# Kernel optimization log

Measured on AMD Instinct MI355X. Metric: run time of the kernel, lower is better.

The kernel has to match this reference:

```python
import jax, jax.numpy as jnp
import numpy as np

N_NODES = 10000
N_EDGES = 50000
N_GRAPHS = 64
NODE_DIM = 32
EDGE_DIM = 16
HID = 64
EDGE_HID = 128
OUT_DIM = 1
T_STEPS = 3       # message-passing rounds
S2S_STEPS = 6     # Set2Set processing steps


def setup_inputs() -> dict:
    key = jax.random.key(0)
    ks = jax.random.split(key, 24)
    def w(k, shape, scale):
        return (jax.random.normal(k, shape, dtype=jnp.float32) * scale)
    inp = {}
    inp["node_features"] = jax.random.normal(ks[0], (N_NODES, NODE_DIM), dtype=jnp.float32)
    inp["edge_features"] = jax.random.normal(ks[1], (N_EDGES, EDGE_DIM), dtype=jnp.float32)
    inp["edge_index"] = jax.random.randint(ks[2], (2, N_EDGES), 0, N_NODES, dtype=jnp.int32)
    # sorted, fully-covering graph assignment (nodes of each graph are contiguous)
    inp["batch_indices"] = ((jnp.arange(N_NODES) * N_GRAPHS) // N_NODES).astype(jnp.int32)
    # input projection
    inp["W_proj"] = w(ks[3], (NODE_DIM, HID), 1.0 / np.sqrt(NODE_DIM))
    inp["b_proj"] = jnp.zeros((HID,), jnp.float32)
    # edge network MLP: edge_dim -> edge_hid -> hid*hid
    inp["W_e1"] = w(ks[4], (EDGE_DIM, EDGE_HID), 1.0 / np.sqrt(EDGE_DIM))
    inp["b_e1"] = jnp.zeros((EDGE_HID,), jnp.float32)
    inp["W_e2"] = w(ks[5], (EDGE_HID, HID * HID), 0.01)
    inp["b_e2"] = jnp.zeros((HID * HID,), jnp.float32)
    # GRU cell (torch layout: 3*hid rows = r,z,n)
    inp["W_gih"] = w(ks[6], (3 * HID, HID), 1.0 / np.sqrt(HID))
    inp["W_ghh"] = w(ks[7], (3 * HID, HID), 1.0 / np.sqrt(HID))
    inp["b_gih"] = jnp.zeros((3 * HID,), jnp.float32)
    inp["b_ghh"] = jnp.zeros((3 * HID,), jnp.float32)
    # LSTM cell (torch layout: 4*hid rows = i,f,g,o), input 2*hid
    inp["W_lih"] = w(ks[8], (4 * HID, 2 * HID), 1.0 / np.sqrt(HID))
    inp["W_lhh"] = w(ks[9], (4 * HID, HID), 1.0 / np.sqrt(HID))
    inp["b_lih"] = jnp.zeros((4 * HID,), jnp.float32)
    inp["b_lhh"] = jnp.zeros((4 * HID,), jnp.float32)
    # readout MLP: 2*hid -> hid -> out
    inp["W_m1"] = w(ks[10], (2 * HID, HID), 1.0 / np.sqrt(2 * HID))
    inp["b_m1"] = jnp.zeros((HID,), jnp.float32)
    inp["W_m2"] = w(ks[11], (HID, OUT_DIM), 1.0 / np.sqrt(HID))
    inp["b_m2"] = jnp.zeros((OUT_DIM,), jnp.float32)
    return inp


def _scatter_softmax(e, idx, n_seg):
    mx = jax.ops.segment_max(e, idx, num_segments=n_seg)
    ex = jnp.exp(e - mx[idx])
    s = jax.ops.segment_sum(ex, idx, num_segments=n_seg)
    return ex / (s[idx] + 1e-16)


def _mpnn_forward(node_features, edge_features, edge_index, batch_indices,
                  W_proj, b_proj, W_e1, b_e1, W_e2, b_e2,
                  W_gih, W_ghh, b_gih, b_ghh,
                  W_lih, W_lhh, b_lih, b_lhh,
                  W_m1, b_m1, W_m2, b_m2):
    n_nodes = node_features.shape[0]
    dst = edge_index[0]  # receiving node v
    src = edge_index[1]  # sending node w

    # input projection
    h = node_features @ W_proj + b_proj                       # (N, H)

    # edge network: per-edge transformation matrix A(e_vw) (depends only on edge feats)
    A = jax.nn.relu(edge_features @ W_e1 + b_e1) @ W_e2 + b_e2
    A = A.reshape(-1, HID, HID)                               # (E, H, H)

    # T rounds: gather senders, per-edge bmm, scatter-add to receivers, GRU update
    for _ in range(T_STEPS):
        msgs = jnp.einsum('eij,ej->ei', A, h[src])            # (E, H)
        m = jax.ops.segment_sum(msgs, dst, num_segments=n_nodes)
        gx = m @ W_gih.T + b_gih                              # (N, 3H)
        gh = h @ W_ghh.T + b_ghh
        xr, xz, xn = jnp.split(gx, 3, axis=-1)
        hr, hz, hn = jnp.split(gh, 3, axis=-1)
        r = jax.nn.sigmoid(xr + hr)
        z = jax.nn.sigmoid(xz + hz)
        n = jnp.tanh(xn + r * hn)
        h = (1.0 - z) * n + z * h

    # Set2Set readout
    hs = jnp.zeros((N_GRAPHS, HID), h.dtype)
    cs = jnp.zeros((N_GRAPHS, HID), h.dtype)
    rs = jnp.zeros((N_GRAPHS, HID), h.dtype)
    for _ in range(S2S_STEPS):
        q = hs[batch_indices]                                 # (N, H)
        e = jnp.sum(h * q, axis=-1)                           # (N,)
        a = _scatter_softmax(e, batch_indices, N_GRAPHS)
        rs = jax.ops.segment_sum(a[:, None] * h, batch_indices, num_segments=N_GRAPHS)
        x = jnp.concatenate([hs, rs], axis=-1)                # (G, 2H)
        gates = x @ W_lih.T + b_lih + hs @ W_lhh.T + b_lhh    # (G, 4H)
        i, f, g, o = jnp.split(gates, 4, axis=-1)
        cs = jax.nn.sigmoid(f) * cs + jax.nn.sigmoid(i) * jnp.tanh(g)
        hs = jax.nn.sigmoid(o) * jnp.tanh(cs)
    ge = jnp.concatenate([hs, rs], axis=-1)                   # (G, 2H)
    return jax.nn.relu(ge @ W_m1 + b_m1) @ W_m2 + b_m2        # (G, out)


def reference(node_features, edge_features, edge_index, batch_indices,
              W_proj, b_proj, W_e1, b_e1, W_e2, b_e2,
              W_gih, W_ghh, b_gih, b_ghh,
              W_lih, W_lhh, b_lih, b_lhh,
              W_m1, b_m1, W_m2, b_m2):
    return _mpnn_forward(node_features, edge_features, edge_index, batch_indices,
                         W_proj, b_proj, W_e1, b_e1, W_e2, b_e2,
                         W_gih, W_ghh, b_gih, b_ghh,
                         W_lih, W_lhh, b_lih, b_lhh,
                         W_m1, b_m1, W_m2, b_m2)
```

## Files before the change

### kernel.cpp

```cpp
#include <hip/hip_runtime.h>

#define N_NODES   10000
#define N_EDGES   50000
#define N_GRAPHS  64
#define NODE_DIM  32
#define EDGE_DIM  16
#define HID       64
#define EHID      128
#define T_STEPS   3
#define S2S_STEPS 6

typedef _Float16 half_t;
typedef _Float16 f16x8 __attribute__((ext_vector_type(8)));
typedef float    f32x4 __attribute__((ext_vector_type(4)));

__device__ __forceinline__ float sigf(float x){ return 1.0f/(1.0f + expf(-x)); }

__global__ void k_zero(float* p, int n){
  int i = blockIdx.x*256 + threadIdx.x;
  if (i < n) p[i] = 0.0f;
}

__global__ void k_proj(const float* __restrict__ nf, const float* __restrict__ Wp,
                       const float* __restrict__ bp, float* __restrict__ h){
  int idx = blockIdx.x*256 + threadIdx.x;
  if (idx >= N_NODES*HID) return;
  int n = idx >> 6;
  int c = idx & 63;
  float acc = bp[c];
  const float* row = nf + (size_t)n*NODE_DIM;
  for (int j = 0; j < NODE_DIM; ++j)
    acc = fmaf(row[j], Wp[j*HID + c], acc);
  h[idx] = acc;
}

__global__ void k_tw2(const float* __restrict__ W2, float* __restrict__ Mm){
  int idx = blockIdx.x*256 + threadIdx.x;
  if (idx >= 64*8192) return;
  int j = idx >> 13; int o = idx & 8191; int k = o >> 6; int i = o & 63;
  Mm[idx] = W2[(size_t)k*4096 + i*64 + j];
}

__global__ void k_w2bt(const float* __restrict__ W2, half_t* __restrict__ BT){
  int idx = blockIdx.x*256 + threadIdx.x;
  if (idx >= 512*2*64*8) return;
  int j    = idx & 7;
  int lane = (idx >> 3) & 63;
  int tk   = (idx >> 9) & 1;
  int tn   = idx >> 10;
  int k = tk*32 + ((lane >> 4) << 3) + j;
  int o = tn*16 + (lane & 15);
  BT[idx] = (half_t)W2[(size_t)(o >> 6)*4096 + (o & 63)*64 + k];
}

__global__ void k_h2a(const float* __restrict__ h, half_t* __restrict__ AT){
  int idx = blockIdx.x*256 + threadIdx.x;
  if (idx >= 625*2*64*8) return;
  int j    = idx & 7;
  int lane = (idx >> 3) & 63;
  int tk   = (idx >> 9) & 1;
  int tm   = idx >> 10;
  int mrow = tm*16 + (lane & 15);
  int k    = tk*32 + ((lane >> 4) << 3) + j;
  AT[idx] = (half_t)h[(size_t)mrow*64 + k];
}

__global__ void k_prep(const float* __restrict__ h, const float* __restrict__ be2,
                       float* __restrict__ m, float* __restrict__ bhp,
                       half_t* __restrict__ AT){
  int idx = blockIdx.x*256 + threadIdx.x;
  if (idx >= N_NODES*HID) return;
  m[idx] = 0.0f;
  int n = idx >> 6, i = idx & 63;
  float acc = 0.0f;
  const float* row = be2 + (size_t)i*64;
  const float* hr  = h + (size_t)n*64;
  for (int j = 0; j < 64; ++j)
    acc = fmaf(row[j], hr[j], acc);
  bhp[idx] = acc;
  int j    = idx & 7;
  int lane = (idx >> 3) & 63;
  int tk   = (idx >> 9) & 1;
  int tm   = idx >> 10;
  int mrow = tm*16 + (lane & 15);
  int k    = tk*32 + ((lane >> 4) << 3) + j;
  AT[idx] = (half_t)h[(size_t)mrow*64 + k];
}

__global__ void k_twg(const float* __restrict__ Wg, const float* __restrict__ Wh,
                      float* __restrict__ WgT, float* __restrict__ WhT){
  int idx = blockIdx.x*256 + threadIdx.x;
  if (idx >= 192*64) return;
  int row = idx >> 6;
  int j   = idx & 63;
  WgT[j*192 + row] = Wg[(size_t)row*64 + j];
  WhT[j*192 + row] = Wh[(size_t)row*64 + j];
}

__global__ void k_ehid(const float* __restrict__ ef, const float* __restrict__ W1,
                       const float* __restrict__ b1, float* __restrict__ Hid){
  int idx = blockIdx.x*256 + threadIdx.x;
  if (idx >= N_EDGES*EHID) return;
  int e = idx >> 7, c = idx & 127;
  float acc = b1[c];
  const float* er = ef + (size_t)e*EDGE_DIM;
  for (int j = 0; j < EDGE_DIM; ++j)
    acc = fmaf(er[j], W1[j*EHID + c], acc);
  Hid[idx] = fmaxf(acc, 0.0f);
}

__global__ void k_ehid16(const float* __restrict__ ef, const float* __restrict__ W1,
                         const float* __restrict__ b1, half_t* __restrict__ Hid16){
  int idx = blockIdx.x*256 + threadIdx.x;
  if (idx >= N_EDGES*EHID) return;
  int e = idx >> 7, c = idx & 127;
  float acc = b1[c];
  const float* er = ef + (size_t)e*EDGE_DIM;
  for (int j = 0; j < EDGE_DIM; ++j)
    acc = fmaf(er[j], W1[j*EHID + c], acc);
  Hid16[idx] = (half_t)fmaxf(acc, 0.0f);
}

__global__ void k_bh(const float* __restrict__ h, const float* __restrict__ be2,
                     float* __restrict__ bh){
  int idx = blockIdx.x*256 + threadIdx.x;
  if (idx >= N_NODES*HID) return;
  int n = idx >> 6, i = idx & 63;
  float acc = 0.0f;
  const float* row = be2 + (size_t)i*64;
  const float* hr  = h + (size_t)n*64;
  for (int j = 0; j < 64; ++j)
    acc = fmaf(row[j], hr[j], acc);
  bh[idx] = acc;
}

__global__ void k_hist(const int* __restrict__ ei, int* __restrict__ deg){
  int e = blockIdx.x*256 + threadIdx.x;
  if (e >= N_EDGES) return;
  atomicAdd(&deg[ei[N_EDGES + e]], 1);
}

__global__ void k_scan(const int* __restrict__ deg, int* __restrict__ rowptr,
                       int* __restrict__ cursor){
  __shared__ int part[256];
  int t = threadIdx.x;
  int base = t*40;
  int s = 0;
  for (int i = 0; i < 40; ++i){
    int idx = base + i;
    if (idx < N_NODES) s += deg[idx];
  }
  part[t] = s;
  __syncthreads();
  for (int off = 1; off < 256; off <<= 1){
    int v = (t >= off) ? part[t - off] : 0;
    __syncthreads();
    part[t] += v;
    __syncthreads();
  }
  int run = (t > 0) ? part[t - 1] : 0;
  for (int i = 0; i < 40; ++i){
    int idx = base + i;
    if (idx < N_NODES){
      rowptr[idx] = run;
      cursor[idx] = run;
      run += deg[idx];
    }
  }
  if (t == 255) rowptr[N_NODES] = run;
}

__global__ void k_scatter(const int* __restrict__ ei, int* __restrict__ cursor,
                          int* __restrict__ csr){
  int e = blockIdx.x*256 + threadIdx.x;
  if (e >= N_EDGES) return;
  int src = ei[N_EDGES + e];
  int pos = atomicAdd(&cursor[src], 1);
  csr[pos] = e;
}

__global__ void MPNN_55705725829535_kernel(const half_t* __restrict__ AT,
                                           const half_t* __restrict__ BT,
                                           const int* __restrict__ rowptr,
                                           const int* __restrict__ csr,
                                           const int* __restrict__ ei,
                                           const half_t* __restrict__ Hid16,
                                           const float* __restrict__ bh,
                                           float* __restrict__ m){
  __shared__ half_t Ct[8][4][520];
  __shared__ int dstW[4][16];
  int wv   = threadIdx.x >> 6;
  int lane = threadIdx.x & 63;
  int quad = lane >> 4;
  int colb = lane & 15;
  int tmb = blockIdx.x;
  int q   = blockIdx.y;
  int tile = tmb >> 1;
  int hi   = tmb & 1;

  int srcl = (lane & 48) | (hi << 3) | (lane & 7);
  const f16x8* Ab = (const f16x8*)AT + (size_t)tile*128;
  f16x8 a0 = Ab[srcl];
  f16x8 a1 = Ab[64 + srcl];
  #pragma unroll
  for (int kt = 0; kt < 4; ++kt){
    f32x4 acc[8];
    #pragma unroll
    for (int jj = 0; jj < 8; ++jj){
      acc[jj][0]=0.f; acc[jj][1]=0.f; acc[jj][2]=0.f; acc[jj][3]=0.f;
    }
    #pragma unroll
    for (int jj = 0; jj < 8; ++jj){
      int ke = kt*32 + wv*8 + jj;
      int tn = ke*4 + q;
      const f16x8* Bb = (const f16x8*)BT + (size_t)tn*128;
      acc[jj] = __builtin_amdgcn_mfma_f32_16x16x32_f16(a0, Bb[lane],      acc[jj], 0, 0, 0);
      acc[jj] = __builtin_amdgcn_mfma_f32_16x16x32_f16(a1, Bb[64 + lane], acc[jj], 0, 0, 0);
    }
    if (quad < 2){
      #pragma unroll
      for (int r = 0; r < 4; ++r){
        int node = quad*4 + r;
        f16x8 v;
        #pragma unroll
        for (int jj = 0; jj < 8; ++jj) v[jj] = (half_t)acc[jj][r];
        *(f16x8*)&Ct[node][kt][(wv*16 + colb)*8] = v;
      }
    }
  }
  __syncthreads();

  for (int c = 0; c < 2; ++c){
    int node = wv*2 + c;
    int s = tmb*8 + node;
    int beg  = rowptr[s];
    int endp = rowptr[s + 1];
    if (beg == endp) continue;
    f16x8 B[4];
    #pragma unroll
    for (int kt = 0; kt < 4; ++kt)
      B[kt] = *(const f16x8*)&Ct[node][kt][lane*8];
    float bhc = bh[(size_t)s*64 + q*16 + colb];
    for (int gbeg = beg; gbeg < endp; gbeg += 16){
      int gn = endp - gbeg; if (gn > 16) gn = 16;
      if (lane < 16)
        dstW[wv][lane] = (lane < gn) ? ei[csr[gbeg + lane]] : -1;
      f16x8 A[4];
      if (colb < gn){
        int e = csr[gbeg + colb];
        const f16x8* Hb = (const f16x8*)(Hid16 + (size_t)e*128) + quad;
        #pragma unroll
        for (int kt = 0; kt < 4; ++kt)
          A[kt] = Hb[kt*4];
      } else {
        #pragma unroll
        for (int kt = 0; kt < 4; ++kt)
          #pragma unroll
          for (int p = 0; p < 8; ++p) A[kt][p] = (half_t)0;
      }
      f32x4 acc;
      acc[0]=0.f; acc[1]=0.f; acc[2]=0.f; acc[3]=0.f;
      #pragma unroll
      for (int kt = 0; kt < 4; ++kt)
        acc = __builtin_amdgcn_mfma_f32_16x16x32_f16(A[kt], B[kt], acc, 0, 0, 0);
      #pragma unroll
      for (int r = 0; r < 4; ++r){
        int jrow = quad*4 + r;
        if (jrow < gn){
          int d = dstW[wv][jrow];
          atomicAdd(&m[(size_t)d*64 + q*16 + colb], acc[r] + bhc);
        }
      }
    }
  }
}

__global__ void k_cgemm(const float* __restrict__ h, const float* __restrict__ Mm,
                        half_t* __restrict__ C, int lo, int hi){
  __shared__ float hs[16][64];
  int n0 = lo + blockIdx.x*16;
  int o0 = blockIdx.y*256 + threadIdx.x;
  for (int idx = threadIdx.x; idx < 16*64; idx += 256){
    int nn = idx >> 6, j = idx & 63;
    int node = n0 + nn;
    hs[nn][j] = (node < hi) ? h[(size_t)node*64 + j] : 0.0f;
  }
  __syncthreads();
  float acc0[16], acc1[16];
  #pragma unroll
  for (int nn = 0; nn < 16; ++nn){ acc0[nn] = 0.0f; acc1[nn] = 0.0f; }
  for (int j4 = 0; j4 < 16; ++j4){
    const float* M0 = Mm + (size_t)(j4*4)*8192;
    float a0 = M0[o0],            b0 = M0[o0 + 4096];
    float a1 = M0[8192 + o0],     b1 = M0[8192 + o0 + 4096];
    float a2 = M0[2*8192 + o0],   b2 = M0[2*8192 + o0 + 4096];
    float a3 = M0[3*8192 + o0],   b3 = M0[3*8192 + o0 + 4096];
    #pragma unroll
    for (int nn = 0; nn < 16; ++nn){
      float4 hv = *(const float4*)&hs[nn][j4*4];
      acc0[nn] = fmaf(hv.x, a0, acc0[nn]);
      acc1[nn] = fmaf(hv.x, b0, acc1[nn]);
      acc0[nn] = fmaf(hv.y, a1, acc0[nn]);
      acc1[nn] = fmaf(hv.y, b1, acc1[nn]);
      acc0[nn] = fmaf(hv.z, a2, acc0[nn]);
      acc1[nn] = fmaf(hv.z, b2, acc1[nn]);
      acc0[nn] = fmaf(hv.w, a3, acc0[nn]);
      acc1[nn] = fmaf(hv.w, b3, acc1[nn]);
    }
  }
  #pragma unroll
  for (int nn = 0; nn < 16; ++nn){
    int node = n0 + nn;
    if (node < hi){
      half_t* Cr = C + (size_t)(node - lo)*8192;
      Cr[o0]        = (half_t)acc0[nn];
      Cr[o0 + 4096] = (half_t)acc1[nn];
    }
  }
}

__global__ void k_msg_csr(const int* __restrict__ rowptr,
                          const int* __restrict__ csr,
                          const int* __restrict__ ei,
                          const float* __restrict__ Hid,
                          const half_t* __restrict__ C,
                          const float* __restrict__ bh,
                          float* __restrict__ m, int lo, int hi){
  __shared__ float hidL[4][8][128];
  int wave = threadIdx.x >> 6;
  int lane = threadIdx.x & 63;
  int s = lo + blockIdx.x*4 + wave;
  if (s >= hi) return;
  int beg = rowptr[s];
  int endp = rowptr[s + 1];
  if (beg == endp) return;
  float bhv = bh[(size_t)s*64 + lane];
  const half_t* Cb = C + (size_t)(s - lo)*8192 + lane;
  float (*hl)[128] = hidL[wave];
  for (int gbeg = beg; gbeg < endp; gbeg += 8){
    int gn = endp - gbeg; if (gn > 8) gn = 8;
    int dsts[8];
    int e0 = csr[gbeg];
    #pragma unroll
    for (int j = 0; j < 8; ++j){
      int e = (j < gn) ? csr[gbeg + j] : e0;
      dsts[j] = ei[e];
      hl[j][lane]      = Hid[(size_t)e*128 + lane];
      hl[j][lane + 64] = Hid[(size_t)e*128 + 64 + lane];
    }
    float acc[8];
    #pragma unroll
    for (int j = 0; j < 8; ++j) acc[j] = 0.0f;
    #pragma unroll 4
    for (int k = 0; k < 128; ++k){
      float c = (float)Cb[k*64];
      #pragma unroll
      for (int j = 0; j < 8; ++j)
        acc[j] = fmaf(hl[j][k], c, acc[j]);
    }
    for (int j = 0; j < gn; ++j)
      atomicAdd(&m[(size_t)dsts[j]*64 + lane], acc[j] + bhv);
  }
}

__global__ void k_msg_fb(const int* __restrict__ ei, const float* __restrict__ ef,
                         const float* __restrict__ W1, const float* __restrict__ b1,
                         const float* __restrict__ W2, const float* __restrict__ be2,
                         const float* __restrict__ h, float* __restrict__ m){
  __shared__ float HidL[EHID];
  __shared__ __align__(16) float hsL[HID];
  int e = blockIdx.x;
  int t = threadIdx.x;
  int src = ei[N_EDGES + e];
  int dst = ei[e];
  {
    float a0 = b1[t];
    float a1 = b1[t + 64];
    const float* er = ef + (size_t)e*EDGE_DIM;
    for (int j = 0; j < EDGE_DIM; ++j){
      float ev = er[j];
      a0 = fmaf(ev, W1[j*EHID + t],      a0);
      a1 = fmaf(ev, W1[j*EHID + t + 64], a1);
    }
    HidL[t]      = fmaxf(a0, 0.0f);
    HidL[t + 64] = fmaxf(a1, 0.0f);
    hsL[t] = h[(size_t)src*64 + t];
  }
  __syncthreads();
  float acc = 0.0f;
  for (int k = 0; k < EHID; ++k){
    float s = HidL[k];
    if (s != 0.0f){
      const float* w = W2 + (size_t)k*4096 + t*64;
      float partial = 0.0f;
      for (int j = 0; j < 64; ++j)
        partial = fmaf(hsL[j], w[j], partial);
      acc = fmaf(s, partial, acc);
    }
  }
  {
    const float* w = be2 + (size_t)t*64;
    for (int j = 0; j < 64; ++j)
      acc = fmaf(hsL[j], w[j], acc);
  }
  atomicAdd(&m[(size_t)dst*64 + t], acc);
}

__global__ void k_gru(float* __restrict__ h, const float* __restrict__ m,
                      const float* __restrict__ WgT, const float* __restrict__ WhT,
                      const float* __restrict__ bg, const float* __restrict__ bhb){
  __shared__ float mld[16][64];
  __shared__ float hld[16][64];
  int t  = threadIdx.x;
  int i  = t & 63;
  int wv = t >> 6;
  int n0 = blockIdx.x*16;
  for (int idx = t; idx < 16*64; idx += 256){
    int nn = idx >> 6, j = idx & 63;
    int node = n0 + nn;
    mld[nn][j] = m[(size_t)node*64 + j];
    hld[nn][j] = h[(size_t)node*64 + j];
  }
  __syncthreads();
  float xr[4], xz[4], xn[4], hr[4], hz[4], hn[4];
  #pragma unroll
  for (int c = 0; c < 4; ++c){
    xr[c] = bg[i];  xz[c] = bg[64 + i];  xn[c] = bg[128 + i];
    hr[c] = bhb[i]; hz[c] = bhb[64 + i]; hn[c] = bhb[128 + i];
  }
  for (int j = 0; j < 64; ++j){
    const float* wg = WgT + j*192;
    const float* wh = WhT + j*192;
    float wgr = wg[i], wgz = wg[64 + i], wgn = wg[128 + i];
    float whr = wh[i], whz = wh[64 + i], whn = wh[128 + i];
    #pragma unroll
    for (int c = 0; c < 4; ++c){
      int nn = wv*4 + c;
      float mj = mld[nn][j];
      float hj = hld[nn][j];
      xr[c] = fmaf(mj, wgr, xr[c]);
      xz[c] = fmaf(mj, wgz, xz[c]);
      xn[c] = fmaf(mj, wgn, xn[c]);
      hr[c] = fmaf(hj, whr, hr[c]);
      hz[c] = fmaf(hj, whz, hz[c]);
      hn[c] = fmaf(hj, whn, hn[c]);
    }
  }
  #pragma unroll
  for (int c = 0; c < 4; ++c){
    int nn = wv*4 + c;
    float r  = sigf(xr[c] + hr[c]);
    float z  = sigf(xz[c] + hz[c]);
    float nv = tanhf(xn[c] + r*hn[c]);
    h[(size_t)(n0 + nn)*64 + i] = (1.0f - z)*nv + z*hld[nn][i];
  }
}

__global__ void k_s2s(const float* __restrict__ h,
                      const float* __restrict__ Wli, const float* __restrict__ Wlh,
                      const float* __restrict__ bli, const float* __restrict__ blh,
                      const float* __restrict__ Wm1, const float* __restrict__ bm1,
                      const float* __restrict__ Wm2, const float* __restrict__ bm2,
                      float* __restrict__ out){
  __shared__ float hc[157*65];
  __shared__ float ea[160];
  __shared__ float x[192];
  __shared__ float gpart[512];
  __shared__ float rsp[8][64];
  __shared__ float wredA[8];
  __shared__ float wredB[8];
  __shared__ float hsb[64];
  __shared__ float csb[64];
  __shared__ float rsb[64];
  int g = blockIdx.x;
  int t = threadIdx.x;
  int lane = t & 63;
  int wv   = t >> 6;
  int start = (g*N_NODES + 63) >> 6;
  int end   = ((g + 1)*N_NODES + 63) >> 6;
  int cnt = end - start;
  const float* hg = h + (size_t)start*64;
  for (int idx = t; idx < cnt*64; idx += 512)
    hc[(idx >> 6)*65 + (idx & 63)] = hg[idx];
  if (t < 64){ hsb[t] = 0.0f; csb[t] = 0.0f; rsb[t] = 0.0f; }
  __syncthreads();
  for (int step = 0; step < S2S_STEPS; ++step){
    float ev = -1e30f;
    if (t < cnt){
      float a = 0.0f;
      const float* hr = &hc[t*65];
      for (int i = 0; i < 64; ++i) a = fmaf(hr[i], hsb[i], a);
      ev = a;
    }
    float v = ev;
    for (int o = 32; o > 0; o >>= 1) v = fmaxf(v, __shfl_xor(v, o));
    if (lane == 0) wredA[wv] = v;
    __syncthreads();
    float mx = wredA[0];
    #pragma unroll
    for (int i = 1; i < 8; ++i) mx = fmaxf(mx, wredA[i]);
    float ex = (t < cnt) ? expf(ev - mx) : 0.0f;
    float sv = ex;
    for (int o = 32; o > 0; o >>= 1) sv += __shfl_xor(sv, o);
    if (lane == 0) wredB[wv] = sv;
    __syncthreads();
    float ssum = 0.0f;
    #pragma unroll
    for (int i = 0; i < 8; ++i) ssum += wredB[i];
    if (t < cnt) ea[t] = ex / (ssum + 1e-16f);
    __syncthreads();
    {
      int n0 = wv*20;
      int n1 = n0 + 20; if (n1 > cnt) n1 = cnt;
      float r = 0.0f;
      for (int n = n0; n < n1; ++n)
        r = fmaf(ea[n], hc[n*65 + lane], r);
      rsp[wv][lane] = r;
    }
    __syncthreads();
    if (t < 64){
      float r = rsp[0][t] + rsp[1][t] + rsp[2][t] + rsp[3][t]
              + rsp[4][t] + rsp[5][t] + rsp[6][t] + rsp[7][t];
      rsb[t] = r;
      x[t]        = hsb[t];
      x[64 + t]   = r;
      x[128 + t]  = hsb[t];
    }
    __syncthreads();
    {
      int gate = t & 255;
      int half = t >> 8;
      float gl = 0.0f;
      if (half == 0){
        const float* wr = Wli + (size_t)gate*128;
        for (int jj = 0; jj < 96; ++jj) gl = fmaf(x[jj], wr[jj], gl);
      } else {
        const float* wr = Wli + (size_t)gate*128;
        for (int jj = 96; jj < 128; ++jj) gl = fmaf(x[jj], wr[jj], gl);
        const float* wh = Wlh + (size_t)gate*64;
        for (int jj = 0; jj < 64; ++jj) gl = fmaf(x[128 + jj], wh[jj], gl);
      }
      gpart[t] = gl;
    }
    __syncthreads();
    if (t < 64){
      float iv = sigf (gpart[t]       + gpart[t + 256]       + bli[t]       + blh[t]);
      float fv = sigf (gpart[64 + t]  + gpart[64 + t + 256]  + bli[64 + t]  + blh[64 + t]);
      float gv = tanhf(gpart[128 + t] + gpart[128 + t + 256] + bli[128 + t] + blh[128 + t]);
      float ov = sigf (gpart[192 + t] + gpart[192 + t + 256] + bli[192 + t] + blh[192 + t]);
      float c  = fv*csb[t] + iv*gv;
      csb[t] = c;
      hsb[t] = ov*tanhf(c);
    }
    __syncthreads();
  }
  float rv = 0.0f;
  if (t < 64){
    float v = bm1[t];
    for (int j = 0; j < 64; ++j) v = fmaf(hsb[j], Wm1[(size_t)j*64 + t],        v);
    for (int j = 0; j < 64; ++j) v = fmaf(rsb[j], Wm1[(size_t)(64 + j)*64 + t], v);
    v = fmaxf(v, 0.0f);
    rv = v * Wm2[t];
  }
  for (int o = 32; o > 0; o >>= 1) rv += __shfl_xor(rv, o);
  if (lane == 0) wredA[wv] = rv;
  __syncthreads();
  if (t == 0) out[g] = wredA[0] + wredA[1] + wredA[2] + wredA[3]
                     + wredA[4] + wredA[5] + wredA[6] + wredA[7] + bm2[0];
}

extern "C" void kernel_launch(void* const* d_in, const int* in_sizes, int n_in,
                              void* d_out, int out_size, void* d_ws, size_t ws_size,
                              hipStream_t stream){
  (void)in_sizes; (void)n_in; (void)out_size;

  const float* nf  = (const float*)d_in[0];
  const float* ef  = (const float*)d_in[1];
  const int*   ei  = (const int*)d_in[2];
  const float* Wp  = (const float*)d_in[4];
  const float* bp  = (const float*)d_in[5];
  const float* We1 = (const float*)d_in[6];
  const float* be1 = (const float*)d_in[7];
  const float* We2 = (const float*)d_in[8];
  const float* be2 = (const float*)d_in[9];
  const float* Wg  = (const float*)d_in[10];
  const float* Wh  = (const float*)d_in[11];
  const float* bg  = (const float*)d_in[12];
  const float* bhb = (const float*)d_in[13];
  const float* Wli = (const float*)d_in[14];
  const float* Wlh = (const float*)d_in[15];
  const float* bli = (const float*)d_in[16];
  const float* blh = (const float*)d_in[17];
  const float* Wm1 = (const float*)d_in[18];
  const float* bm1 = (const float*)d_in[19];
  const float* Wm2 = (const float*)d_in[20];
  const float* bm2 = (const float*)d_in[21];

  float* out = (float*)d_out;
  float* ws  = (float*)d_ws;

  float* h    = ws;
  float* m    = ws + 640000;
  float* bh   = ws + 1280000;
  float* Mm   = ws + 1920000;
  float* WgT  = ws + 2444288;
  float* WhT  = ws + 2456576;
  float* Hid  = ws + 2468864;
  half_t* Hid16 = (half_t*)Hid;
  int*   deg    = (int*)(ws + 8868864);
  int*   rowptr = deg + 10000;
  int*   cursor = rowptr + 10001;
  int*   csr    = cursor + 10000;
  half_t* AT  = (half_t*)(ws + 8948880);
  half_t* BT  = (half_t*)(ws + 9268880);
  const size_t C_OFF = 9531024;
  half_t* C   = (half_t*)(ws + C_OFF);

  long long c_halves = ((long long)ws_size - (long long)C_OFF*4) / 2;
  int NC = (c_halves > 0) ? (int)(c_halves / 8192) : 0;
  if (NC > N_NODES) NC = N_NODES;
  int use_c_path = (NC >= 512);
  int use_mfma   = (NC >= N_NODES);

  k_proj<<<(N_NODES*HID + 255)/256, 256, 0, stream>>>(nf, Wp, bp, h);

  if (use_c_path){
    k_twg <<<(192*64 + 255)/256, 256, 0, stream>>>(Wg, Wh, WgT, WhT);
    k_zero<<<(10000 + 255)/256, 256, 0, stream>>>((float*)deg, 10000);
    k_hist<<<(N_EDGES + 255)/256, 256, 0, stream>>>(ei, deg);
    k_scan<<<1, 256, 0, stream>>>(deg, rowptr, cursor);
    k_scatter<<<(N_EDGES + 255)/256, 256, 0, stream>>>(ei, cursor, csr);
    if (use_mfma){
      k_ehid16<<<(N_EDGES*EHID + 255)/256, 256, 0, stream>>>(ef, We1, be1, Hid16);
      k_w2bt<<<(512*2*64*8 + 255)/256, 256, 0, stream>>>(We2, BT);
      for (int step = 0; step < T_STEPS; ++step){
        k_prep<<<(N_NODES*HID + 255)/256, 256, 0, stream>>>(h, be2, m, bh, AT);
        dim3 grid(1250, 4);
        MPNN_55705725829535_kernel<<<grid, 256, 0, stream>>>(
            AT, BT, rowptr, csr, ei, Hid16, bh, m);
        k_gru<<<625, 256, 0, stream>>>(h, m, WgT, WhT, bg, bhb);
      }
    } else {
      k_ehid<<<(N_EDGES*EHID + 255)/256, 256, 0, stream>>>(ef, We1, be1, Hid);
      k_tw2<<<(64*8192)/256, 256, 0, stream>>>(We2, Mm);
      for (int step = 0; step < T_STEPS; ++step){
        k_zero<<<(N_NODES*HID + 255)/256, 256, 0, stream>>>(m, N_NODES*HID);
        k_bh<<<(N_NODES*HID + 255)/256, 256, 0, stream>>>(h, be2, bh);
        for (int lo = 0; lo < N_NODES; lo += NC){
          int hi = (lo + NC < N_NODES) ? lo + NC : N_NODES;
          int cnt = hi - lo;
          dim3 grid((cnt + 15)/16, 16);
          k_cgemm<<<grid, 256, 0, stream>>>(h, Mm, C, lo, hi);
          k_msg_csr<<<(cnt + 3)/4, 256, 0, stream>>>(
              rowptr, csr, ei, Hid, C, bh, m, lo, hi);
        }
        k_gru<<<625, 256, 0, stream>>>(h, m, WgT, WhT, bg, bhb);
      }
    }
  } else {
    k_twg <<<(192*64 + 255)/256, 256, 0, stream>>>(Wg, Wh, WgT, WhT);
    for (int step = 0; step < T_STEPS; ++step){
      k_zero<<<(N_NODES*HID + 255)/256, 256, 0, stream>>>(m, N_NODES*HID);
      k_msg_fb<<<N_EDGES, 64, 0, stream>>>(ei, ef, We1, be1, We2, be2, h, m);
      k_gru<<<625, 256, 0, stream>>>(h, m, WgT, WhT, bg, bhb);
    }
  }
  k_s2s<<<N_GRAPHS, 512, 0, stream>>>(h, Wli, Wlh, bli, blh,
                                      Wm1, bm1, Wm2, bm2, out);
}
```

Before: 582.6 us.

## Split message kernel over K halves, using full 16-node MFMA tiles per block

```diff
diff --git a/kernel.cpp b/kernel.cpp
--- a/kernel.cpp
+++ b/kernel.cpp
@@ -187,23 +187,22 @@
                                            const half_t* __restrict__ Hid16,
                                            const float* __restrict__ bh,
                                            float* __restrict__ m){
-  __shared__ half_t Ct[8][4][520];
+  __shared__ half_t Ct[16][2][520];
   __shared__ int dstW[4][16];
   int wv   = threadIdx.x >> 6;
   int lane = threadIdx.x & 63;
   int quad = lane >> 4;
   int colb = lane & 15;
-  int tmb = blockIdx.x;
-  int q   = blockIdx.y;
-  int tile = tmb >> 1;
-  int hi   = tmb & 1;
-
-  int srcl = (lane & 48) | (hi << 3) | (lane & 7);
-  const f16x8* Ab = (const f16x8*)AT + (size_t)tile*128;
-  f16x8 a0 = Ab[srcl];
-  f16x8 a1 = Ab[64 + srcl];
+  int tm = blockIdx.x;
+  int q  = blockIdx.y;
+  int kh = blockIdx.z;
+
+  const f16x8* Ab = (const f16x8*)AT + (size_t)tm*128;
+  f16x8 a0 = Ab[lane];
+  f16x8 a1 = Ab[64 + lane];
   #pragma unroll
-  for (int kt = 0; kt < 4; ++kt){
+  for (int ktl = 0; ktl < 2; ++ktl){
+    int kt = kh*2 + ktl;
     f32x4 acc[8];
     #pragma unroll
     for (int jj = 0; jj < 8; ++jj){
@@ -217,52 +216,44 @@
       acc[jj] = __builtin_amdgcn_mfma_f32_16x16x32_f16(a0, Bb[lane],      acc[jj], 0, 0, 0);
       acc[jj] = __builtin_amdgcn_mfma_f32_16x16x32_f16(a1, Bb[64 + lane], acc[jj], 0, 0, 0);
     }
-    if (quad < 2){
+    #pragma unroll
+    for (int r = 0; r < 4; ++r){
+      int node = quad*4 + r;
+      f16x8 v;
       #pragma unroll
-      for (int r = 0; r < 4; ++r){
-        int node = quad*4 + r;
-        f16x8 v;
-        #pragma unroll
-        for (int jj = 0; jj < 8; ++jj) v[jj] = (half_t)acc[jj][r];
-        *(f16x8*)&Ct[node][kt][(wv*16 + colb)*8] = v;
-      }
+      for (int jj = 0; jj < 8; ++jj) v[jj] = (half_t)acc[jj][r];
+      *(f16x8*)&Ct[node][ktl][(wv*16 + colb)*8] = v;
     }
   }
   __syncthreads();
 
-  for (int c = 0; c < 2; ++c){
-    int node = wv*2 + c;
-    int s = tmb*8 + node;
+  for (int c = 0; c < 4; ++c){
+    int node = wv*4 + c;
+    int s = tm*16 + node;
     int beg  = rowptr[s];
     int endp = rowptr[s + 1];
     if (beg == endp) continue;
-    f16x8 B[4];
-    #pragma unroll
-    for (int kt = 0; kt < 4; ++kt)
-      B[kt] = *(const f16x8*)&Ct[node][kt][lane*8];
-    float bhc = bh[(size_t)s*64 + q*16 + colb];
+    f16x8 B0 = *(const f16x8*)&Ct[node][0][lane*8];
+    f16x8 B1 = *(const f16x8*)&Ct[node][1][lane*8];
+    float bhc = (kh == 0) ? bh[(size_t)s*64 + q*16 + colb] : 0.0f;
     for (int gbeg = beg; gbeg < endp; gbeg += 16){
       int gn = endp - gbeg; if (gn > 16) gn = 16;
       if (lane < 16)
         dstW[wv][lane] = (lane < gn) ? ei[csr[gbeg + lane]] : -1;
-      f16x8 A[4];
+      f16x8 A0, A1;
       if (colb < gn){
         int e = csr[gbeg + colb];
         const f16x8* Hb = (const f16x8*)(Hid16 + (size_t)e*128) + quad;
-        #pragma unroll
-        for (int kt = 0; kt < 4; ++kt)
-          A[kt] = Hb[kt*4];
+        A0 = Hb[(kh*2 + 0)*4];
+        A1 = Hb[(kh*2 + 1)*4];
       } else {
         #pragma unroll
-        for (int kt = 0; kt < 4; ++kt)
-          #pragma unroll
-          for (int p = 0; p < 8; ++p) A[kt][p] = (half_t)0;
+        for (int p = 0; p < 8; ++p){ A0[p] = (half_t)0; A1[p] = (half_t)0; }
       }
       f32x4 acc;
       acc[0]=0.f; acc[1]=0.f; acc[2]=0.f; acc[3]=0.f;
-      #pragma unroll
-      for (int kt = 0; kt < 4; ++kt)
-        acc = __builtin_amdgcn_mfma_f32_16x16x32_f16(A[kt], B[kt], acc, 0, 0, 0);
+      acc = __builtin_amdgcn_mfma_f32_16x16x32_f16(A0, B0, acc, 0, 0, 0);
+      acc = __builtin_amdgcn_mfma_f32_16x16x32_f16(A1, B1, acc, 0, 0, 0);
       #pragma unroll
       for (int r = 0; r < 4; ++r){
         int jrow = quad*4 + r;
@@ -635,7 +626,7 @@
       k_w2bt<<<(512*2*64*8 + 255)/256, 256, 0, stream>>>(We2, BT);
       for (int step = 0; step < T_STEPS; ++step){
         k_prep<<<(N_NODES*HID + 255)/256, 256, 0, stream>>>(h, be2, m, bh, AT);
-        dim3 grid(1250, 4);
+        dim3 grid(625, 4, 2);
         MPNN_55705725829535_kernel<<<grid, 256, 0, stream>>>(
             AT, BT, rowptr, csr, ei, Hid16, bh, m);
         k_gru<<<625, 256, 0, stream>>>(h, m, WgT, WhT, bg, bhb);
```

New measurement: 580.8 us. About the same (-0.3%).
